# Kernel tuning notes

Hardware: AMD Instinct MI355X
Metric: run time of the kernel (lower is better)

## Reference

```python
import jax, jax.numpy as jnp
import numpy as np

N_ML, N_MM, L = 128, 8192, 60.0

def _half_shifts():
    # torchani _get_shifts half-shift enumeration for num_repeats=(1,1,1)
    r, o, m = [1], [0], [-1]
    def cp(a, b, c):
        return [(x, y, z) for x in a for y in b for z in c]
    combos = (cp(r, r, r) + cp(r, r, o) + cp(r, r, m)
              + cp(r, o, r) + cp(r, o, o) + cp(r, o, m)
              + cp(r, m, r) + cp(r, m, o) + cp(r, m, m)
              + cp(o, r, r) + cp(o, r, o) + cp(o, r, m)
              + cp(o, o, r))
    return np.array(combos, dtype=np.int32)  # (13, 3)

def setup_inputs() -> dict:
    key = jax.random.key(0)
    positions = jax.random.uniform(key, (N_ML + N_MM, 3), dtype=jnp.float32) * L
    cell = jnp.eye(3, dtype=jnp.float32) * L
    cutoffs = jnp.array([10.0, 14.0], dtype=jnp.float32)
    shifts = jnp.asarray(_half_shifts())              # (S=13, 3) int32
    ml_idx = jnp.arange(N_ML, dtype=jnp.int32)        # fragment 0 atoms
    mm_idx = jnp.arange(N_ML, N_ML + N_MM, dtype=jnp.int32)  # fragment 1 atoms
    return {"positions": positions, "cell": cell, "cutoffs": cutoffs,
            "shifts": shifts, "ml_idx": ml_idx, "mm_idx": mm_idx}

def reference(positions, cell, cutoffs, shifts, ml_idx, mm_idx):
    n_ml, n_mm = ml_idx.shape[0], mm_idx.shape[0]
    S = shifts.shape[0]
    # center image (zero shift) + periodic half-shifts -> (S+1, 3)
    shift_frac = jnp.concatenate(
        [jnp.zeros((1, 3), positions.dtype), shifts.astype(positions.dtype)], axis=0)
    shift_vec = shift_frac @ cell                     # (S+1, 3) cartesian
    # cartesian product ML x MM (matches torch.cartesian_prod ordering: sorted by i)
    pi = jnp.broadcast_to(ml_idx[:, None], (n_ml, n_mm)).reshape(-1)  # (P0,)
    pj = jnp.broadcast_to(mm_idx[None, :], (n_ml, n_mm)).reshape(-1)  # (P0,)
    # Rij = pos[i] - pos[j] + shift @ cell over all images: (S+1, P0, 3)
    Rij = positions[pi][None, :, :] - positions[pj][None, :, :] + shift_vec[:, None, :]
    d2 = jnp.sum(Rij * Rij, axis=-1).reshape(-1)      # (P,) P=(S+1)*P0
    P = d2.shape[0]
    pi_all = jnp.broadcast_to(pi[None, :], (S + 1, pi.shape[0])).reshape(-1)
    pj_all = jnp.broadcast_to(pj[None, :], (S + 1, pj.shape[0])).reshape(-1)
    sf_all = jnp.broadcast_to(shift_frac[:, None, :], (S + 1, pi.shape[0], 3)).reshape(-1, 3)
    # bi-directional duplication: bi_offset = cat((-seg_offset, seg_offset))
    idx_i = jnp.concatenate([pi_all, pj_all])          # (2P,)
    idx_j = jnp.concatenate([pj_all, pi_all])          # (2P,)
    offsets_frac = jnp.concatenate([-sf_all, sf_all], axis=0)  # (2P, 3)
    offsets_cart = offsets_frac @ cell                 # (2P, 3), seg_offset @ cell
    d2_full = jnp.concatenate([d2, d2])                # |Rij| symmetric under i<->j
    # per-cutoff in-range masks (fixed-shape stand-in for dynamic index compaction)
    masks = d2_full[None, :] < (cutoffs ** 2)[:, None]  # (n_cutoffs, 2P) bool
    return idx_i, idx_j, offsets_cart, d2_full, masks
```

## Files before the change

### kernel.cpp

```cpp
#include <hip/hip_runtime.h>
#include <stdint.h>

typedef float f4 __attribute__((ext_vector_type(4)));

__device__ __forceinline__ f4 rot3(float x, float y, float z, int t) {
    float a0 = (t == 0) ? x : ((t == 1) ? y : z);
    float a1 = (t == 0) ? y : ((t == 1) ? z : x);
    float a2 = (t == 0) ? z : ((t == 1) ? x : y);
    f4 r = {a0, a1, a2, a0};
    return r;
}

__global__ __launch_bounds__(256) void nl_kernel(
    const float* __restrict__ pos,
    const float* __restrict__ cell,
    const float* __restrict__ cutoffs,
    const int*   __restrict__ shifts,
    const int*   __restrict__ ml_idx,
    const int*   __restrict__ mm_idx,
    float* __restrict__ out,
    int n_mm, int P0, int P)
{
    int tid = blockIdx.x * blockDim.x + threadIdx.x;
    int p = tid << 2;
    if (p >= P) return;

    int s     = p / P0;
    int a     = p - s * P0;
    int i_idx = a / n_mm;
    int j0    = a - i_idx * n_mm;

    int pi = ml_idx[i_idx];
    float xi = pos[3 * pi + 0], yi = pos[3 * pi + 1], zi = pos[3 * pi + 2];

    int sx = 0, sy = 0, sz = 0;
    if (s > 0) {
        sx = shifts[3 * (s - 1) + 0];
        sy = shifts[3 * (s - 1) + 1];
        sz = shifts[3 * (s - 1) + 2];
    }
    float fx = (float)sx, fy = (float)sy, fz = (float)sz;
    float svx = __fadd_rn(__fadd_rn(__fmul_rn(fx, cell[0]), __fmul_rn(fy, cell[3])), __fmul_rn(fz, cell[6]));
    float svy = __fadd_rn(__fadd_rn(__fmul_rn(fx, cell[1]), __fmul_rn(fy, cell[4])), __fmul_rn(fz, cell[7]));
    float svz = __fadd_rn(__fadd_rn(__fmul_rn(fx, cell[2]), __fmul_rn(fy, cell[5])), __fmul_rn(fz, cell[8]));

    float c0 = __fmul_rn(cutoffs[0], cutoffs[0]);
    float c1 = __fmul_rn(cutoffs[1], cutoffs[1]);

    float fI = (float)pi;
    f4 vI = {fI, fI, fI, fI};
    f4 vJ, vD, vM0, vM1;

    int4 pj4 = *(const int4*)(mm_idx + j0);
    int pjs[4] = {pj4.x, pj4.y, pj4.z, pj4.w};
#pragma unroll
    for (int k = 0; k < 4; ++k) {
        int pj = pjs[k];
        float xj = pos[3 * pj + 0], yj = pos[3 * pj + 1], zj = pos[3 * pj + 2];
        float dx = __fadd_rn(__fsub_rn(xi, xj), svx);
        float dy = __fadd_rn(__fsub_rn(yi, yj), svy);
        float dz = __fadd_rn(__fsub_rn(zi, zj), svz);
        float d2 = __fadd_rn(__fadd_rn(__fmul_rn(dx, dx), __fmul_rn(dy, dy)), __fmul_rn(dz, dz));
        vJ[k]  = (float)pj;
        vD[k]  = d2;
        vM0[k] = (d2 < c0) ? 1.0f : 0.0f;
        vM1[k] = (d2 < c1) ? 1.0f : 0.0f;
    }

    size_t Pz = (size_t)P;
    size_t pp = (size_t)p;
    *(f4*)(out + 0 * Pz + pp)  = vI;
    *(f4*)(out + 1 * Pz + pp)  = vJ;
    *(f4*)(out + 2 * Pz + pp)  = vJ;
    *(f4*)(out + 3 * Pz + pp)  = vI;
    *(f4*)(out + 10 * Pz + pp) = vD;
    *(f4*)(out + 11 * Pz + pp) = vD;
    *(f4*)(out + 12 * Pz + pp) = vM0;
    *(f4*)(out + 13 * Pz + pp) = vM0;
    *(f4*)(out + 14 * Pz + pp) = vM1;
    *(f4*)(out + 15 * Pz + pp) = vM1;

    int lane = (int)(threadIdx.x & 63);
    size_t pw = pp - (size_t)(lane << 2);
    float nx = -svx, ny = -svy, nz = -svz;
    float* nb = out + 4 * Pz + 3 * pw;
    float* qb = out + 7 * Pz + 3 * pw;

    if (pw + 256 <= (size_t)P) {
#pragma unroll
        for (int c = 0; c < 3; ++c) {
            int t = (lane + c) % 3;
            *(f4*)(nb + c * 256 + 4 * lane) = rot3(nx, ny, nz, t);
            *(f4*)(qb + c * 256 + 4 * lane) = rot3(svx, svy, svz, t);
        }
    } else {
        float* n0 = out + 4 * Pz + 3 * pp;
        float* q0 = out + 7 * Pz + 3 * pp;
#pragma unroll
        for (int r = 0; r < 4; ++r) {
            n0[3*r+0] = nx;  n0[3*r+1] = ny;  n0[3*r+2] = nz;
            q0[3*r+0] = svx; q0[3*r+1] = svy; q0[3*r+2] = svz;
        }
    }
}

extern "C" void kernel_launch(void* const* d_in, const int* in_sizes, int n_in,
                              void* d_out, int out_size, void* d_ws, size_t ws_size,
                              hipStream_t stream) {
    const float* pos    = (const float*)d_in[0];
    const float* cell   = (const float*)d_in[1];
    const float* cut    = (const float*)d_in[2];
    const int*   shifts = (const int*)d_in[3];
    const int*   ml     = (const int*)d_in[4];
    const int*   mm     = (const int*)d_in[5];

    int n_ml = in_sizes[4];
    int n_mm = in_sizes[5];
    int S    = in_sizes[3] / 3;
    int P0   = n_ml * n_mm;
    int P    = (S + 1) * P0;

    int threads = P / 4;
    int grid = (threads + 255) / 256;
    nl_kernel<<<grid, 256, 0, stream>>>(pos, cell, cut, shifts, ml, mm,
                                        (float*)d_out, n_mm, P0, P);
}
```

Measured before the change: 910.1 us.

## Split output writes by plane so each block writes one contiguous output region

The work is reorganized so that each block handles a single output plane (16 planes of size P), and each thread writes 16 contiguous floats instead of scattering 4-float stores across ten planes plus interleaved offset planes. The goal is write streams that are fully contiguous per wavefront and avoid mixing many distant store targets. The cost is redundant distance computation: the d2 and mask planes each recompute the distance, six times in total instead of once, and index math such as modulo and division is now done per plane.

```diff
diff --git a/kernel.cpp b/kernel.cpp
--- a/kernel.cpp
+++ b/kernel.cpp
@@ -19,87 +19,96 @@
     const int*   __restrict__ ml_idx,
     const int*   __restrict__ mm_idx,
     float* __restrict__ out,
-    int n_mm, int P0, int P)
+    int n_mm, int P0, int P, int blocks_per_sub)
 {
-    int tid = blockIdx.x * blockDim.x + threadIdx.x;
-    int p = tid << 2;
+    int sub = blockIdx.x / blocks_per_sub;
+    int rb  = blockIdx.x - sub * blocks_per_sub;
+    int u   = rb * blockDim.x + (int)threadIdx.x;
+    int p   = u << 4;
     if (p >= P) return;
 
-    int s     = p / P0;
-    int a     = p - s * P0;
-    int i_idx = a / n_mm;
-    int j0    = a - i_idx * n_mm;
+    float* dst = out + (size_t)sub * (size_t)P + (size_t)p;
 
-    int pi = ml_idx[i_idx];
-    float xi = pos[3 * pi + 0], yi = pos[3 * pi + 1], zi = pos[3 * pi + 2];
-
-    int sx = 0, sy = 0, sz = 0;
-    if (s > 0) {
-        sx = shifts[3 * (s - 1) + 0];
-        sy = shifts[3 * (s - 1) + 1];
-        sz = shifts[3 * (s - 1) + 2];
-    }
-    float fx = (float)sx, fy = (float)sy, fz = (float)sz;
-    float svx = __fadd_rn(__fadd_rn(__fmul_rn(fx, cell[0]), __fmul_rn(fy, cell[3])), __fmul_rn(fz, cell[6]));
-    float svy = __fadd_rn(__fadd_rn(__fmul_rn(fx, cell[1]), __fmul_rn(fy, cell[4])), __fmul_rn(fz, cell[7]));
-    float svz = __fadd_rn(__fadd_rn(__fmul_rn(fx, cell[2]), __fmul_rn(fy, cell[5])), __fmul_rn(fz, cell[8]));
-
-    float c0 = __fmul_rn(cutoffs[0], cutoffs[0]);
-    float c1 = __fmul_rn(cutoffs[1], cutoffs[1]);
-
-    float fI = (float)pi;
-    f4 vI = {fI, fI, fI, fI};
-    f4 vJ, vD, vM0, vM1;
-
-    int4 pj4 = *(const int4*)(mm_idx + j0);
-    int pjs[4] = {pj4.x, pj4.y, pj4.z, pj4.w};
+    if (sub == 0 || sub == 3) {
+        int a = p % P0;
+        int pi = ml_idx[a / n_mm];
+        float fI = (float)pi;
+        f4 v = {fI, fI, fI, fI};
+        f4* o = (f4*)dst;
+        o[0] = v; o[1] = v; o[2] = v; o[3] = v;
+    } else if (sub == 1 || sub == 2) {
+        int a = p % P0;
+        int j0 = a % n_mm;
+        f4* o = (f4*)dst;
 #pragma unroll
-    for (int k = 0; k < 4; ++k) {
-        int pj = pjs[k];
-        float xj = pos[3 * pj + 0], yj = pos[3 * pj + 1], zj = pos[3 * pj + 2];
-        float dx = __fadd_rn(__fsub_rn(xi, xj), svx);
-        float dy = __fadd_rn(__fsub_rn(yi, yj), svy);
-        float dz = __fadd_rn(__fsub_rn(zi, zj), svz);
-        float d2 = __fadd_rn(__fadd_rn(__fmul_rn(dx, dx), __fmul_rn(dy, dy)), __fmul_rn(dz, dz));
-        vJ[k]  = (float)pj;
-        vD[k]  = d2;
-        vM0[k] = (d2 < c0) ? 1.0f : 0.0f;
-        vM1[k] = (d2 < c1) ? 1.0f : 0.0f;
-    }
-
-    size_t Pz = (size_t)P;
-    size_t pp = (size_t)p;
-    *(f4*)(out + 0 * Pz + pp)  = vI;
-    *(f4*)(out + 1 * Pz + pp)  = vJ;
-    *(f4*)(out + 2 * Pz + pp)  = vJ;
-    *(f4*)(out + 3 * Pz + pp)  = vI;
-    *(f4*)(out + 10 * Pz + pp) = vD;
-    *(f4*)(out + 11 * Pz + pp) = vD;
-    *(f4*)(out + 12 * Pz + pp) = vM0;
-    *(f4*)(out + 13 * Pz + pp) = vM0;
-    *(f4*)(out + 14 * Pz + pp) = vM1;
-    *(f4*)(out + 15 * Pz + pp) = vM1;
-
-    int lane = (int)(threadIdx.x & 63);
-    size_t pw = pp - (size_t)(lane << 2);
-    float nx = -svx, ny = -svy, nz = -svz;
-    float* nb = out + 4 * Pz + 3 * pw;
-    float* qb = out + 7 * Pz + 3 * pw;
-
-    if (pw + 256 <= (size_t)P) {
+        for (int g = 0; g < 4; ++g) {
+            int4 pj4 = *(const int4*)(mm_idx + j0 + 4 * g);
+            f4 v = {(float)pj4.x, (float)pj4.y, (float)pj4.z, (float)pj4.w};
+            o[g] = v;
+        }
+    } else if (sub >= 4 && sub <= 9) {
+        int q = (sub - 4) * P + p;
+        int P3 = 3 * P;
+        int neg = (q < P3);
+        int q2 = neg ? q : (q - P3);
+        int row = q2 / 3;
+        int s = row / P0;
+        int sx = 0, sy = 0, sz = 0;
+        if (s > 0) {
+            sx = shifts[3 * (s - 1) + 0];
+            sy = shifts[3 * (s - 1) + 1];
+            sz = shifts[3 * (s - 1) + 2];
+        }
+        float fx = (float)sx, fy = (float)sy, fz = (float)sz;
+        float svx = __fadd_rn(__fadd_rn(__fmul_rn(fx, cell[0]), __fmul_rn(fy, cell[3])), __fmul_rn(fz, cell[6]));
+        float svy = __fadd_rn(__fadd_rn(__fmul_rn(fx, cell[1]), __fmul_rn(fy, cell[4])), __fmul_rn(fz, cell[7]));
+        float svz = __fadd_rn(__fadd_rn(__fmul_rn(fx, cell[2]), __fmul_rn(fy, cell[5])), __fmul_rn(fz, cell[8]));
+        if (neg) { svx = -svx; svy = -svy; svz = -svz; }
+        int t0 = q2 % 3;
+        f4* o = (f4*)dst;
 #pragma unroll
-        for (int c = 0; c < 3; ++c) {
-            int t = (lane + c) % 3;
-            *(f4*)(nb + c * 256 + 4 * lane) = rot3(nx, ny, nz, t);
-            *(f4*)(qb + c * 256 + 4 * lane) = rot3(svx, svy, svz, t);
+        for (int c = 0; c < 4; ++c) {
+            int t = (t0 + 4 * c) % 3;
+            o[c] = rot3(svx, svy, svz, t);
         }
     } else {
-        float* n0 = out + 4 * Pz + 3 * pp;
-        float* q0 = out + 7 * Pz + 3 * pp;
+        int s = p / P0;
+        int a = p - s * P0;
+        int i_idx = a / n_mm;
+        int j0 = a - i_idx * n_mm;
+        int pi = ml_idx[i_idx];
+        float xi = pos[3 * pi + 0], yi = pos[3 * pi + 1], zi = pos[3 * pi + 2];
+        int sx = 0, sy = 0, sz = 0;
+        if (s > 0) {
+            sx = shifts[3 * (s - 1) + 0];
+            sy = shifts[3 * (s - 1) + 1];
+            sz = shifts[3 * (s - 1) + 2];
+        }
+        float fx = (float)sx, fy = (float)sy, fz = (float)sz;
+        float svx = __fadd_rn(__fadd_rn(__fmul_rn(fx, cell[0]), __fmul_rn(fy, cell[3])), __fmul_rn(fz, cell[6]));
+        float svy = __fadd_rn(__fadd_rn(__fmul_rn(fx, cell[1]), __fmul_rn(fy, cell[4])), __fmul_rn(fz, cell[7]));
+        float svz = __fadd_rn(__fadd_rn(__fmul_rn(fx, cell[2]), __fmul_rn(fy, cell[5])), __fmul_rn(fz, cell[8]));
+
+        bool is_d2 = (sub < 12);
+        float cc = (sub < 14) ? __fmul_rn(cutoffs[0], cutoffs[0])
+                              : __fmul_rn(cutoffs[1], cutoffs[1]);
+        f4* o = (f4*)dst;
 #pragma unroll
-        for (int r = 0; r < 4; ++r) {
-            n0[3*r+0] = nx;  n0[3*r+1] = ny;  n0[3*r+2] = nz;
-            q0[3*r+0] = svx; q0[3*r+1] = svy; q0[3*r+2] = svz;
+        for (int g = 0; g < 4; ++g) {
+            int4 pj4 = *(const int4*)(mm_idx + j0 + 4 * g);
+            int pjs[4] = {pj4.x, pj4.y, pj4.z, pj4.w};
+            f4 v;
+#pragma unroll
+            for (int k = 0; k < 4; ++k) {
+                int pj = pjs[k];
+                float xj = pos[3 * pj + 0], yj = pos[3 * pj + 1], zj = pos[3 * pj + 2];
+                float dx = __fadd_rn(__fsub_rn(xi, xj), svx);
+                float dy = __fadd_rn(__fsub_rn(yi, yj), svy);
+                float dz = __fadd_rn(__fsub_rn(zi, zj), svz);
+                float d2 = __fadd_rn(__fadd_rn(__fmul_rn(dx, dx), __fmul_rn(dy, dy)), __fmul_rn(dz, dz));
+                v[k] = is_d2 ? d2 : ((d2 < cc) ? 1.0f : 0.0f);
+            }
+            o[g] = v;
         }
     }
 }
@@ -120,8 +129,9 @@
     int P0   = n_ml * n_mm;
     int P    = (S + 1) * P0;
 
-    int threads = P / 4;
-    int grid = (threads + 255) / 256;
+    int threads_per_sub = P / 16;
+    int blocks_per_sub  = (threads_per_sub + 255) / 256;
+    int grid = 16 * blocks_per_sub;
     nl_kernel<<<grid, 256, 0, stream>>>(pos, cell, cut, shifts, ml, mm,
-                                        (float*)d_out, n_mm, P0, P);
+                                        (float*)d_out, n_mm, P0, P, blocks_per_sub);
 }
```

Measured after the change: 1.082 ms. +18.8%, slower.

## Split output writing into specialized block roles for distance, index and offset planes

Applied to the files above, without the earlier changes.

The single fused kernel becomes three block roles in one grid: compute blocks write the distance and mask planes, index blocks write the i/j index planes, and offset blocks each write 16 contiguous floats of the offset planes, rebuilding shift vectors from the flat index. The goal is to shrink per-thread register and work imbalance and to give the store-heavy offset region wide contiguous vector writes in place of the rotated per-lane pattern. The cost is redundant index arithmetic, shift-vector recomputation in every offset thread, and more blocks to launch.

```diff
diff --git a/kernel.cpp b/kernel.cpp
--- a/kernel.cpp
+++ b/kernel.cpp
@@ -11,6 +11,22 @@
     return r;
 }
 
+__device__ __forceinline__ void shift_vec(
+    const float* __restrict__ cell, const int* __restrict__ shifts, int s,
+    float& svx, float& svy, float& svz)
+{
+    int sx = 0, sy = 0, sz = 0;
+    if (s > 0) {
+        sx = shifts[3 * (s - 1) + 0];
+        sy = shifts[3 * (s - 1) + 1];
+        sz = shifts[3 * (s - 1) + 2];
+    }
+    float fx = (float)sx, fy = (float)sy, fz = (float)sz;
+    svx = __fadd_rn(__fadd_rn(__fmul_rn(fx, cell[0]), __fmul_rn(fy, cell[3])), __fmul_rn(fz, cell[6]));
+    svy = __fadd_rn(__fadd_rn(__fmul_rn(fx, cell[1]), __fmul_rn(fy, cell[4])), __fmul_rn(fz, cell[7]));
+    svz = __fadd_rn(__fadd_rn(__fmul_rn(fx, cell[2]), __fmul_rn(fy, cell[5])), __fmul_rn(fz, cell[8]));
+}
+
 __global__ __launch_bounds__(256) void nl_kernel(
     const float* __restrict__ pos,
     const float* __restrict__ cell,
@@ -19,88 +35,87 @@
     const int*   __restrict__ ml_idx,
     const int*   __restrict__ mm_idx,
     float* __restrict__ out,
-    int n_mm, int P0, int P)
+    int n_mm, int P0, int P, int nC, int nA, int bps16)
 {
-    int tid = blockIdx.x * blockDim.x + threadIdx.x;
-    int p = tid << 2;
-    if (p >= P) return;
+    size_t Pz = (size_t)P;
+    int b = blockIdx.x;
 
-    int s     = p / P0;
-    int a     = p - s * P0;
-    int i_idx = a / n_mm;
-    int j0    = a - i_idx * n_mm;
+    if (b < nC + nA) {
+        bool isC = (b < nC);
+        int cb = isC ? b : (b - nC);
+        int p = (cb << 10) + ((int)threadIdx.x << 2);
+        if (p >= P) return;
+        size_t pp = (size_t)p;
 
-    int pi = ml_idx[i_idx];
-    float xi = pos[3 * pi + 0], yi = pos[3 * pi + 1], zi = pos[3 * pi + 2];
+        int s     = p / P0;
+        int a     = p - s * P0;
+        int i_idx = a / n_mm;
+        int j0    = a - i_idx * n_mm;
+        int4 pj4  = *(const int4*)(mm_idx + j0);
 
-    int sx = 0, sy = 0, sz = 0;
-    if (s > 0) {
-        sx = shifts[3 * (s - 1) + 0];
-        sy = shifts[3 * (s - 1) + 1];
-        sz = shifts[3 * (s - 1) + 2];
-    }
-    float fx = (float)sx, fy = (float)sy, fz = (float)sz;
-    float svx = __fadd_rn(__fadd_rn(__fmul_rn(fx, cell[0]), __fmul_rn(fy, cell[3])), __fmul_rn(fz, cell[6]));
-    float svy = __fadd_rn(__fadd_rn(__fmul_rn(fx, cell[1]), __fmul_rn(fy, cell[4])), __fmul_rn(fz, cell[7]));
-    float svz = __fadd_rn(__fadd_rn(__fmul_rn(fx, cell[2]), __fmul_rn(fy, cell[5])), __fmul_rn(fz, cell[8]));
+        if (!isC) {
+            float fI = (float)ml_idx[i_idx];
+            f4 vI = {fI, fI, fI, fI};
+            f4 vJ = {(float)pj4.x, (float)pj4.y, (float)pj4.z, (float)pj4.w};
+            *(f4*)(out + 0 * Pz + pp) = vI;
+            *(f4*)(out + 1 * Pz + pp) = vJ;
+            *(f4*)(out + 2 * Pz + pp) = vJ;
+            *(f4*)(out + 3 * Pz + pp) = vI;
+            return;
+        }
 
-    float c0 = __fmul_rn(cutoffs[0], cutoffs[0]);
-    float c1 = __fmul_rn(cutoffs[1], cutoffs[1]);
+        int pi = ml_idx[i_idx];
+        float xi = pos[3 * pi + 0], yi = pos[3 * pi + 1], zi = pos[3 * pi + 2];
+        float svx, svy, svz;
+        shift_vec(cell, shifts, s, svx, svy, svz);
+        float c0 = __fmul_rn(cutoffs[0], cutoffs[0]);
+        float c1 = __fmul_rn(cutoffs[1], cutoffs[1]);
 
-    float fI = (float)pi;
-    f4 vI = {fI, fI, fI, fI};
-    f4 vJ, vD, vM0, vM1;
-
-    int4 pj4 = *(const int4*)(mm_idx + j0);
-    int pjs[4] = {pj4.x, pj4.y, pj4.z, pj4.w};
+        int pjs[4] = {pj4.x, pj4.y, pj4.z, pj4.w};
+        f4 vD, vM0, vM1;
 #pragma unroll
-    for (int k = 0; k < 4; ++k) {
-        int pj = pjs[k];
-        float xj = pos[3 * pj + 0], yj = pos[3 * pj + 1], zj = pos[3 * pj + 2];
-        float dx = __fadd_rn(__fsub_rn(xi, xj), svx);
-        float dy = __fadd_rn(__fsub_rn(yi, yj), svy);
-        float dz = __fadd_rn(__fsub_rn(zi, zj), svz);
-        float d2 = __fadd_rn(__fadd_rn(__fmul_rn(dx, dx), __fmul_rn(dy, dy)), __fmul_rn(dz, dz));
-        vJ[k]  = (float)pj;
-        vD[k]  = d2;
-        vM0[k] = (d2 < c0) ? 1.0f : 0.0f;
-        vM1[k] = (d2 < c1) ? 1.0f : 0.0f;
+        for (int k = 0; k < 4; ++k) {
+            int pj = pjs[k];
+            float xj = pos[3 * pj + 0], yj = pos[3 * pj + 1], zj = pos[3 * pj + 2];
+            float dx = __fadd_rn(__fsub_rn(xi, xj), svx);
+            float dy = __fadd_rn(__fsub_rn(yi, yj), svy);
+            float dz = __fadd_rn(__fsub_rn(zi, zj), svz);
+            float d2 = __fadd_rn(__fadd_rn(__fmul_rn(dx, dx), __fmul_rn(dy, dy)), __fmul_rn(dz, dz));
+            vD[k]  = d2;
+            vM0[k] = (d2 < c0) ? 1.0f : 0.0f;
+            vM1[k] = (d2 < c1) ? 1.0f : 0.0f;
+        }
+        *(f4*)(out + 10 * Pz + pp) = vD;
+        *(f4*)(out + 11 * Pz + pp) = vD;
+        *(f4*)(out + 12 * Pz + pp) = vM0;
+        *(f4*)(out + 13 * Pz + pp) = vM0;
+        *(f4*)(out + 14 * Pz + pp) = vM1;
+        *(f4*)(out + 15 * Pz + pp) = vM1;
+        return;
     }
 
-    size_t Pz = (size_t)P;
-    size_t pp = (size_t)p;
-    *(f4*)(out + 0 * Pz + pp)  = vI;
-    *(f4*)(out + 1 * Pz + pp)  = vJ;
-    *(f4*)(out + 2 * Pz + pp)  = vJ;
-    *(f4*)(out + 3 * Pz + pp)  = vI;
-    *(f4*)(out + 10 * Pz + pp) = vD;
-    *(f4*)(out + 11 * Pz + pp) = vD;
-    *(f4*)(out + 12 * Pz + pp) = vM0;
-    *(f4*)(out + 13 * Pz + pp) = vM0;
-    *(f4*)(out + 14 * Pz + pp) = vM1;
-    *(f4*)(out + 15 * Pz + pp) = vM1;
+    int b2  = b - nC - nA;
+    int sub = 4 + b2 / bps16;
+    int rb  = b2 - (sub - 4) * bps16;
+    int p   = (rb * (int)blockDim.x + (int)threadIdx.x) << 4;
+    if (p >= P) return;
+    float* dst = out + (size_t)sub * Pz + (size_t)p;
 
-    int lane = (int)(threadIdx.x & 63);
-    size_t pw = pp - (size_t)(lane << 2);
-    float nx = -svx, ny = -svy, nz = -svz;
-    float* nb = out + 4 * Pz + 3 * pw;
-    float* qb = out + 7 * Pz + 3 * pw;
-
-    if (pw + 256 <= (size_t)P) {
+    int q  = (sub - 4) * P + p;
+    int P3 = 3 * P;
+    int neg = (q < P3);
+    int q2 = neg ? q : (q - P3);
+    int row = q2 / 3;
+    int s = row / P0;
+    float svx, svy, svz;
+    shift_vec(cell, shifts, s, svx, svy, svz);
+    if (neg) { svx = -svx; svy = -svy; svz = -svz; }
+    int t0 = q2 % 3;
+    f4* o = (f4*)dst;
 #pragma unroll
-        for (int c = 0; c < 3; ++c) {
-            int t = (lane + c) % 3;
-            *(f4*)(nb + c * 256 + 4 * lane) = rot3(nx, ny, nz, t);
-            *(f4*)(qb + c * 256 + 4 * lane) = rot3(svx, svy, svz, t);
-        }
-    } else {
-        float* n0 = out + 4 * Pz + 3 * pp;
-        float* q0 = out + 7 * Pz + 3 * pp;
-#pragma unroll
-        for (int r = 0; r < 4; ++r) {
-            n0[3*r+0] = nx;  n0[3*r+1] = ny;  n0[3*r+2] = nz;
-            q0[3*r+0] = svx; q0[3*r+1] = svy; q0[3*r+2] = svz;
-        }
+    for (int c = 0; c < 4; ++c) {
+        int t = (t0 + 4 * c) % 3;
+        o[c] = rot3(svx, svy, svz, t);
     }
 }
 
@@ -120,8 +135,12 @@
     int P0   = n_ml * n_mm;
     int P    = (S + 1) * P0;
 
-    int threads = P / 4;
-    int grid = (threads + 255) / 256;
+    int nC    = (P + 1023) >> 10;
+    int nA    = nC;
+    int bps16 = (P / 16 + 255) / 256;
+    int nB    = 6 * bps16;
+    int grid  = nC + nA + nB;
+
     nl_kernel<<<grid, 256, 0, stream>>>(pos, cell, cut, shifts, ml, mm,
-                                        (float*)d_out, n_mm, P0, P);
+                                        (float*)d_out, n_mm, P0, P, nC, nA, bps16);
 }
```

After: 948.8 us. 1.04x slower.
